# Kernel optimization log

Hardware: AMD Instinct MI355X
Metric: run time of the kernel (lower is better)

The kernel has to match this reference:

```python
import jax, jax.numpy as jnp
import numpy as np

WS = (2, 7, 7)    # window_size (t,h,w)
SS = (1, 3, 3)    # shift_size
HEADS = 4


def _rel_pos_index(ws):
    t, h, w = ws
    coords = np.stack(np.meshgrid(np.arange(t), np.arange(h), np.arange(w), indexing='ij'))
    cf = coords.reshape(3, -1)                       # (3, N)
    rc = (cf[:, :, None] - cf[:, None, :]).transpose(1, 2, 0).astype(np.int64)  # (N,N,3)
    rc[:, :, 0] += t - 1
    rc[:, :, 1] += h - 1
    rc[:, :, 2] += w - 1
    rc[:, :, 0] *= (2 * h - 1) * (2 * w - 1)
    rc[:, :, 1] *= (2 * w - 1)
    return rc.sum(-1)                                # (N,N) int


def _compute_mask(Tp, Hp, Wp, ws, ss, dtype):
    img = np.zeros((1, Tp, Hp, Wp, 1), np.float32)
    cnt = 0
    for d in (slice(-ws[0]), slice(-ws[0], -ss[0]), slice(-ss[0], None)):
        for hh in (slice(-ws[1]), slice(-ws[1], -ss[1]), slice(-ss[1], None)):
            for ww in (slice(-ws[2]), slice(-ws[2], -ss[2]), slice(-ss[2], None)):
                img[:, d, hh, ww, :] = cnt
                cnt += 1
    t, h, w = ws
    m = img.reshape(1, Tp // t, t, Hp // h, h, Wp // w, w, 1)
    m = m.transpose(0, 1, 3, 5, 2, 4, 6, 7).reshape(-1, t * h * w)  # (nW, N)
    am = m[:, None, :] - m[:, :, None]
    return jnp.asarray(np.where(am != 0, -100.0, 0.0), dtype)        # (nW, N, N)


def setup_inputs() -> dict:
    key = jax.random.key(0)
    k0, k1, k2, k3 = jax.random.split(key, 4)
    B, T, H, W, C = 2, 16, 56, 56, 128
    x = jax.random.normal(k0, (B, T, H, W, C), jnp.float32)
    qkv_w = jax.random.normal(k1, (3 * C, C), jnp.float32) * (C ** -0.5)
    proj_w = jax.random.normal(k2, (C, C), jnp.float32) * (C ** -0.5)
    proj_b = jnp.zeros((C,), jnp.float32)
    tbl = (2 * WS[0] - 1) * (2 * WS[1] - 1) * (2 * WS[2] - 1)  # 507
    rpb_table = jax.random.normal(k3, (tbl, HEADS), jnp.float32) * 0.02
    return {"x": x, "qkv_w": qkv_w, "proj_w": proj_w, "proj_b": proj_b, "rpb_table": rpb_table}


def _forward(x, qkv_w, proj_w, proj_b, rpb_table):
    B, T, H, W, C = x.shape
    ws, ss = list(WS), list(SS)
    for i, d in enumerate((T, H, W)):
        if d <= ws[i]:
            ws[i] = d
            ss[i] = 0
    t, h, w = ws
    dims = (T, H, W)
    pad = [(ws[i] - dims[i] % ws[i]) % ws[i] for i in range(3)]
    x = jnp.pad(x, ((0, 0), (0, pad[0]), (0, pad[1]), (0, pad[2]), (0, 0)))
    Tp, Hp, Wp = x.shape[1], x.shape[2], x.shape[3]
    shifted = any(s > 0 for s in ss)
    if shifted:
        x = jnp.roll(x, (-ss[0], -ss[1], -ss[2]), (1, 2, 3))
        mask = _compute_mask(Tp, Hp, Wp, ws, ss, x.dtype)  # (nW, N, N)
    else:
        mask = None
    # window partition -> (B_, N, C)
    xw = x.reshape(B, Tp // t, t, Hp // h, h, Wp // w, w, C)
    xw = xw.transpose(0, 1, 3, 5, 2, 4, 6, 7).reshape(-1, t * h * w, C)
    B_, N, _ = xw.shape
    hd = C // HEADS
    scale = hd ** -0.5
    qkv = (xw @ qkv_w.T).reshape(B_, N, 3, HEADS, hd).transpose(2, 0, 3, 1, 4)
    q, k, v = qkv[0] * scale, qkv[1], qkv[2]           # (B_, heads, N, hd)
    attn = jnp.einsum('bhnd,bhmd->bhnm', q, k)
    rpi = _rel_pos_index(tuple(ws))[:N, :N].reshape(-1)
    bias = rpb_table[rpi].reshape(N, N, HEADS).transpose(2, 0, 1)  # (heads, N, N)
    attn = attn + bias[None]
    if mask is not None:
        nW = mask.shape[0]
        attn = attn.reshape(B_ // nW, nW, HEADS, N, N) + mask[None, :, None]
        attn = attn.reshape(-1, HEADS, N, N)
    attn = jax.nn.softmax(attn, axis=-1)
    out = jnp.einsum('bhnm,bhmd->bnhd', attn, v).reshape(B_, N, C)
    out = out @ proj_w.T + proj_b
    # window reverse (faithful to original, including swapped h/w in the view)
    xr = out.reshape(B, Tp // t, Hp // h, Wp // w, t, w, h, C)
    xr = xr.transpose(0, 1, 4, 2, 5, 3, 6, 7).reshape(B, Tp, Hp, Wp, C)
    if shifted:
        xr = jnp.roll(xr, (ss[0], ss[1], ss[2]), (1, 2, 3))
    return xr[:, :T, :H, :W, :]


def reference(x, qkv_w, proj_w, proj_b, rpb_table):
    return _forward(x, qkv_w, proj_w, proj_b, rpb_table)
```

## Files before the change

kernel.cpp:

```cpp
#include <hip/hip_runtime.h>
#include <hip/hip_bf16.h>

typedef __bf16 bf16x8 __attribute__((ext_vector_type(8)));
typedef __bf16 bf16x4 __attribute__((ext_vector_type(4)));
typedef float  f32x4  __attribute__((ext_vector_type(4)));

#define MFMA16(A,B,C) __builtin_amdgcn_mfma_f32_16x16x32_bf16((A),(B),(C),0,0,0)

constexpr int LQ = 0;
constexpr int LK = LQ + 4*112*80;
constexpr int LV = LK + 4*112*80;
constexpr int LP = LV + 4*32*256;
constexpr int LO = LP + 4*16*256;
constexpr int LDS_BYTES = LO + 112*256;

__device__ __forceinline__ bf16x8 cvt8(float4 a, float4 b) {
    bf16x8 r;
    r[0]=(__bf16)a.x; r[1]=(__bf16)a.y; r[2]=(__bf16)a.z; r[3]=(__bf16)a.w;
    r[4]=(__bf16)b.x; r[5]=(__bf16)b.y; r[6]=(__bf16)b.z; r[7]=(__bf16)b.w;
    return r;
}

__global__ void swin_addt_kernel(const float* __restrict__ rpb, float* __restrict__ addT) {
    int idx = blockIdx.x * 256 + threadIdx.x;
    if (idx >= 8*4*112*112) return;
    int i   = idx % 112;
    int j   = (idx / 112) % 112;
    int h   = (idx / (112*112)) & 3;
    int cls = idx / (112*112*4);
    float v;
    if (j >= 98) v = -1e30f;
    else if (i >= 98) v = 0.0f;
    else {
        int ti = i / 49, ri = i % 49, hi = ri / 7, wi = ri % 7;
        int tj = j / 49, rj = j % 49, hj = rj / 7, wj = rj % 7;
        int rel = (ti - tj + 1)*169 + (hi - hj + 6)*13 + (wi - wj + 6);
        v = rpb[rel*4 + h];
        int rt_i = (cls & 4) ? (1 + ti) : 0;
        int rh_i = (cls & 2) ? ((hi < 4) ? 1 : 2) : 0;
        int rw_i = (cls & 1) ? ((wi < 4) ? 1 : 2) : 0;
        int rt_j = (cls & 4) ? (1 + tj) : 0;
        int rh_j = (cls & 2) ? ((hj < 4) ? 1 : 2) : 0;
        int rw_j = (cls & 1) ? ((wj < 4) ? 1 : 2) : 0;
        if (rt_i*9 + rh_i*3 + rw_i != rt_j*9 + rh_j*3 + rw_j) v -= 100.0f;
    }
    addT[idx] = v;
}

__global__ __launch_bounds__(256, 1)
void swin_fused_kernel(const float* __restrict__ x, const float* __restrict__ qkv_w,
                       const float* __restrict__ proj_w, const float* __restrict__ proj_b,
                       const float* __restrict__ addT, float* __restrict__ out) {
    __shared__ __align__(16) unsigned char smem[LDS_BYTES];
    const int tid  = threadIdx.x;
    const int lane = tid & 63;
    const int wv   = tid >> 6;
    const int l15  = lane & 15;
    const int l4   = lane >> 4;

    const int win  = blockIdx.x;
    const int b    = win >> 9;
    const int wr   = win & 511;
    const int bt   = wr >> 6, bh = (wr >> 3) & 7, bw = wr & 7;
    const int cls  = ((bt==7)?4:0) | ((bh==7)?2:0) | ((bw==7)?1:0);

    const f32x4 fz = {0.f, 0.f, 0.f, 0.f};

    for (int i = tid; i < 4*32*16; i += 256) {
        int n  = 112 + (i & 15);
        int d  = (i >> 4) & 31;
        int hh = i >> 9;
        *(__bf16*)(smem + LV + ((hh*32 + d) << 8) + ((2*n) ^ ((d & 7) << 4))) = (__bf16)0.0f;
    }

    bf16x8 wfr[6][4];
    for (int cs = 0; cs < 6; ++cs) {
        int part = cs >> 1;
        int row  = part*128 + wv*32 + ((cs & 1) << 4) + l15;
        const float* wp = qkv_w + row*128 + l4*8;
        for (int ks = 0; ks < 4; ++ks)
            wfr[cs][ks] = cvt8(*(const float4*)(wp + ks*32), *(const float4*)(wp + ks*32 + 4));
    }
    const float kscale = 0.17677669529663687f;
    for (int mt = 0; mt < 7; ++mt) {
        int n  = mt*16 + l15;
        int it = n / 49; int rr = n - it*49; int ih = rr / 7; int iw = rr - ih*7;
        int ts = (bt*2 + it + 1) & 15;
        int hs = bh*7 + ih + 3; if (hs >= 56) hs -= 56;
        int vs = bw*7 + iw + 3; if (vs >= 56) vs -= 56;
        const float* xp = x + (((b*16 + ts)*56 + hs)*56 + vs)*128 + l4*8;
        bf16x8 afr[4];
        for (int ks = 0; ks < 4; ++ks)
            afr[ks] = cvt8(*(const float4*)(xp + ks*32), *(const float4*)(xp + ks*32 + 4));
        f32x4 acc[6];
        for (int cs = 0; cs < 6; ++cs) acc[cs] = fz;
        for (int ks = 0; ks < 4; ++ks)
            for (int cs = 0; cs < 6; ++cs)
                acc[cs] = MFMA16(afr[ks], wfr[cs][ks], acc[cs]);
        for (int cs = 0; cs < 6; ++cs) {
            int part = cs >> 1;
            int d    = ((cs & 1) << 4) + l15;
            for (int r = 0; r < 4; ++r) {
                int nn = mt*16 + l4*4 + r;
                float v = acc[cs][r];
                if (part == 0)
                    *(__bf16*)(smem + LQ + (wv*112 + nn)*80 + d*2) = (__bf16)(v * kscale);
                else if (part == 1)
                    *(__bf16*)(smem + LK + (wv*112 + nn)*80 + d*2) = (__bf16)v;
                else
                    *(__bf16*)(smem + LV + ((wv*32 + d) << 8) + ((2*nn) ^ ((d & 7) << 4))) = (__bf16)v;
            }
        }
    }
    __syncthreads();

    bf16x8 kfr[7];
    for (int nt = 0; nt < 7; ++nt)
        kfr[nt] = *(const bf16x8*)(smem + LK + (wv*112 + nt*16 + l15)*80 + l4*16);
    bf16x8 vfr[4][2];
    for (int ks = 0; ks < 4; ++ks)
        for (int dt = 0; dt < 2; ++dt) {
            int d = dt*16 + l15;
            vfr[ks][dt] = *(const bf16x8*)(smem + LV + ((wv*32 + d) << 8) + ((2*(ks*32 + l4*8)) ^ ((d & 7) << 4)));
        }
    {
        int row = l15, col = 112 + l4*4;
        bf16x4 z4; z4[0]=z4[1]=z4[2]=z4[3]=(__bf16)0.0f;
        *(bf16x4*)(smem + LP + wv*4096 + row*256 + ((2*col) ^ ((row & 7) << 4))) = z4;
    }
    const float* at = addT + (cls*4 + wv)*112*112;
    for (int mt = 0; mt < 7; ++mt) {
        bf16x8 qfr = *(const bf16x8*)(smem + LQ + (wv*112 + mt*16 + l15)*80 + l4*16);
        f32x4 s[7];
        for (int nt = 0; nt < 7; ++nt) s[nt] = MFMA16(qfr, kfr[nt], fz);
        for (int nt = 0; nt < 7; ++nt)
            s[nt] += *(const f32x4*)(at + (nt*16 + l15)*112 + mt*16 + l4*4);
        float mx[4], sum[4];
        for (int r = 0; r < 4; ++r) {
            float m = s[0][r];
            for (int nt = 1; nt < 7; ++nt) m = fmaxf(m, s[nt][r]);
            m = fmaxf(m, __shfl_xor(m, 1));
            m = fmaxf(m, __shfl_xor(m, 2));
            m = fmaxf(m, __shfl_xor(m, 4));
            m = fmaxf(m, __shfl_xor(m, 8));
            mx[r] = m; sum[r] = 0.f;
        }
        for (int nt = 0; nt < 7; ++nt)
            for (int r = 0; r < 4; ++r) {
                float p = __expf(s[nt][r] - mx[r]);
                s[nt][r] = p;
                sum[r]  += p;
            }
        for (int r = 0; r < 4; ++r) {
            sum[r] += __shfl_xor(sum[r], 1);
            sum[r] += __shfl_xor(sum[r], 2);
            sum[r] += __shfl_xor(sum[r], 4);
            sum[r] += __shfl_xor(sum[r], 8);
        }
        for (int nt = 0; nt < 7; ++nt)
            for (int r = 0; r < 4; ++r) {
                int prow = l4*4 + r, pcol = nt*16 + l15;
                *(__bf16*)(smem + LP + wv*4096 + prow*256 + ((2*pcol) ^ ((prow & 7) << 4))) = (__bf16)s[nt][r];
            }
        f32x4 o0 = fz, o1 = fz;
        for (int ks = 0; ks < 4; ++ks) {
            bf16x8 pfr = *(const bf16x8*)(smem + LP + wv*4096 + l15*256 + ((ks*64 + l4*16) ^ ((l15 & 7) << 4)));
            o0 = MFMA16(pfr, vfr[ks][0], o0);
            o1 = MFMA16(pfr, vfr[ks][1], o1);
        }
        for (int r = 0; r < 4; ++r) {
            int nn = mt*16 + l4*4 + r;
            float inv = 1.0f / sum[r];
            int c0 = wv*32 + l15;
            *(__bf16*)(smem + LO + nn*256 + ((2*c0) ^ ((nn & 7) << 4)))      = (__bf16)(o0[r] * inv);
            *(__bf16*)(smem + LO + nn*256 + ((2*(c0+16)) ^ ((nn & 7) << 4))) = (__bf16)(o1[r] * inv);
        }
    }
    __syncthreads();

    bf16x8 pw[2][4];
    float  pb[2];
    for (int nt2 = 0; nt2 < 2; ++nt2) {
        int c = wv*32 + nt2*16 + l15;
        const float* wp = proj_w + c*128 + l4*8;
        for (int ks = 0; ks < 4; ++ks)
            pw[nt2][ks] = cvt8(*(const float4*)(wp + ks*32), *(const float4*)(wp + ks*32 + 4));
        pb[nt2] = proj_b[c];
    }
    for (int mt = 0; mt < 7; ++mt) {
        bf16x8 afr[4];
        int arow = mt*16 + l15;
        for (int ks = 0; ks < 4; ++ks)
            afr[ks] = *(const bf16x8*)(smem + LO + arow*256 + ((ks*64 + l4*16) ^ ((arow & 7) << 4)));
        f32x4 a0 = fz, a1 = fz;
        for (int ks = 0; ks < 4; ++ks) {
            a0 = MFMA16(afr[ks], pw[0][ks], a0);
            a1 = MFMA16(afr[ks], pw[1][ks], a1);
        }
        for (int r = 0; r < 4; ++r) {
            int nn = mt*16 + l4*4 + r;
            if (nn >= 98) continue;
            int it = nn / 49; int rr = nn - it*49; int ih = rr / 7; int iw = rr - ih*7;
            int td = (bt*2 + it + 1) & 15;
            int hd = bh*7 + ih + 3; if (hd >= 56) hd -= 56;
            int wd = bw*7 + iw + 3; if (wd >= 56) wd -= 56;
            float* op = out + (((b*16 + td)*56 + hd)*56 + wd)*128;
            op[wv*32 + l15]      = a0[r] + pb[0];
            op[wv*32 + 16 + l15] = a1[r] + pb[1];
        }
    }
}

extern "C" void kernel_launch(void* const* d_in, const int* in_sizes, int n_in,
                              void* d_out, int out_size, void* d_ws, size_t ws_size,
                              hipStream_t stream) {
    const float* x      = (const float*)d_in[0];
    const float* qkv_w  = (const float*)d_in[1];
    const float* proj_w = (const float*)d_in[2];
    const float* proj_b = (const float*)d_in[3];
    const float* rpb    = (const float*)d_in[4];
    float* out  = (float*)d_out;
    float* addT = (float*)d_ws;

    swin_addt_kernel<<<(8*4*112*112 + 255)/256, 256, 0, stream>>>(rpb, addT);
    swin_fused_kernel<<<1024, 256, 0, stream>>>(x, qkv_w, proj_w, proj_b, addT, out);
}
```

Before: 209.4 us.

## Alias LDS regions and keep Q in registers to fit two blocks per CU

Q tiles are now held in registers during the QKV projection instead of being written to LDS right away. After K and V fragments are loaded and a barrier is passed, Q is written into a region that reuses space freed by K/V, and the P and output buffers overlap the K region. Total LDS drops to 72 KB and launch bounds allow two blocks per CU, aiming to hide latency through higher occupancy. In exchange it adds an extra barrier and more register pressure, since seven Q fragments stay live under a tighter register budget.

Measured after the change: 181.4 us. -13.4%, faster.

```diff
diff --git a/kernel.cpp b/kernel.cpp
--- a/kernel.cpp
+++ b/kernel.cpp
@@ -7,12 +7,12 @@
 
 #define MFMA16(A,B,C) __builtin_amdgcn_mfma_f32_16x16x32_bf16((A),(B),(C),0,0,0)
 
-constexpr int LQ = 0;
-constexpr int LK = LQ + 4*112*80;
-constexpr int LV = LK + 4*112*80;
-constexpr int LP = LV + 4*32*256;
-constexpr int LO = LP + 4*16*256;
-constexpr int LDS_BYTES = LO + 112*256;
+constexpr int LK  = 0;
+constexpr int LV  = 35840;
+constexpr int LP  = 0;
+constexpr int LO  = 16384;
+constexpr int LQS = 45056;
+constexpr int LDS_BYTES = 73728;
 
 __device__ __forceinline__ bf16x8 cvt8(float4 a, float4 b) {
     bf16x8 r;
@@ -47,7 +47,7 @@
     addT[idx] = v;
 }
 
-__global__ __launch_bounds__(256, 1)
+__global__ __launch_bounds__(256, 2)
 void swin_fused_kernel(const float* __restrict__ x, const float* __restrict__ qkv_w,
                        const float* __restrict__ proj_w, const float* __restrict__ proj_b,
                        const float* __restrict__ addT, float* __restrict__ out) {
@@ -82,6 +82,8 @@
             wfr[cs][ks] = cvt8(*(const float4*)(wp + ks*32), *(const float4*)(wp + ks*32 + 4));
     }
     const float kscale = 0.17677669529663687f;
+    bf16x8 q_save[7];
+    #pragma unroll
     for (int mt = 0; mt < 7; ++mt) {
         int n  = mt*16 + l15;
         int it = n / 49; int rr = n - it*49; int ih = rr / 7; int iw = rr - ih*7;
@@ -97,15 +99,21 @@
         for (int ks = 0; ks < 4; ++ks)
             for (int cs = 0; cs < 6; ++cs)
                 acc[cs] = MFMA16(afr[ks], wfr[cs][ks], acc[cs]);
-        for (int cs = 0; cs < 6; ++cs) {
+        bf16x8 qs;
+        #pragma unroll
+        for (int r = 0; r < 4; ++r) {
+            qs[r]     = (__bf16)(acc[0][r] * kscale);
+            qs[r + 4] = (__bf16)(acc[1][r] * kscale);
+        }
+        q_save[mt] = qs;
+        #pragma unroll
+        for (int cs = 2; cs < 6; ++cs) {
             int part = cs >> 1;
             int d    = ((cs & 1) << 4) + l15;
             for (int r = 0; r < 4; ++r) {
                 int nn = mt*16 + l4*4 + r;
                 float v = acc[cs][r];
-                if (part == 0)
-                    *(__bf16*)(smem + LQ + (wv*112 + nn)*80 + d*2) = (__bf16)(v * kscale);
-                else if (part == 1)
+                if (part == 1)
                     *(__bf16*)(smem + LK + (wv*112 + nn)*80 + d*2) = (__bf16)v;
                 else
                     *(__bf16*)(smem + LV + ((wv*32 + d) << 8) + ((2*nn) ^ ((d & 7) << 4))) = (__bf16)v;
@@ -123,6 +131,18 @@
             int d = dt*16 + l15;
             vfr[ks][dt] = *(const bf16x8*)(smem + LV + ((wv*32 + d) << 8) + ((2*(ks*32 + l4*8)) ^ ((d & 7) << 4)));
         }
+    __syncthreads();
+
+    #pragma unroll
+    for (int t = 0; t < 7; ++t) {
+        bf16x8 qs = q_save[t];
+        #pragma unroll
+        for (int e = 0; e < 8; ++e) {
+            int token = l4*4 + (e & 3);
+            int d     = ((e >> 2) << 4) + l15;
+            *(__bf16*)(smem + LQS + wv*7168 + t*1024 + token*64 + d*2) = qs[e];
+        }
+    }
     {
         int row = l15, col = 112 + l4*4;
         bf16x4 z4; z4[0]=z4[1]=z4[2]=z4[3]=(__bf16)0.0f;
@@ -130,7 +150,7 @@
     }
     const float* at = addT + (cls*4 + wv)*112*112;
     for (int mt = 0; mt < 7; ++mt) {
-        bf16x8 qfr = *(const bf16x8*)(smem + LQ + (wv*112 + mt*16 + l15)*80 + l4*16);
+        bf16x8 qfr = *(const bf16x8*)(smem + LQS + wv*7168 + mt*1024 + l15*64 + l4*16);
         f32x4 s[7];
         for (int nt = 0; nt < 7; ++nt) s[nt] = MFMA16(qfr, kfr[nt], fz);
         for (int nt = 0; nt < 7; ++nt)
```
